# Performance work log

Measured on AMD Instinct MI355X. Metric: run time of the kernel, lower is better.

## Reference

```python
import jax, jax.numpy as jnp
import numpy as np

HEADS = 8
EMBED = 64
FEAT_A = 256
FEAT_B = 256


def setup_inputs() -> dict:
    key = jax.random.key(0)
    k1, k2, k3, k4, k5 = jax.random.split(key, 5)
    B, N = 2, 2048
    z_a = jax.random.normal(k1, (B, FEAT_A, N), dtype=jnp.float32)
    z_b = jax.random.normal(k2, (B, FEAT_B, N), dtype=jnp.float32)
    # Conv1d(k=1, bias=False) weights, squeezed: [out_ch, in_ch]
    W_a = jax.random.normal(k3, (HEADS * EMBED, FEAT_A), dtype=jnp.float32) * (1.0 / np.sqrt(FEAT_A))
    W_b = jax.random.normal(k4, (HEADS * EMBED, FEAT_B), dtype=jnp.float32) * (1.0 / np.sqrt(FEAT_B))
    W_c = jax.random.normal(k5, (FEAT_A, HEADS * FEAT_B), dtype=jnp.float32) * (1.0 / np.sqrt(HEADS * FEAT_B))
    return {"z_a": z_a, "z_b": z_b, "W_a": W_a, "W_b": W_b, "W_c": W_c}


def reference(z_a, z_b, W_a, W_b, W_c):
    B, Fa, Na = z_a.shape
    Fb = z_b.shape[1]
    H, E = HEADS, EMBED
    norm = 1.0 / np.sqrt(E)
    # 1x1 conv embeddings -> q, k: [B, H, E, N]
    q = jnp.einsum('of,bfn->bon', W_a, z_a).reshape(B, H, E, Na)
    k = jnp.einsum('of,bfn->bon', W_b, z_b).reshape(B, H, E, -1)
    v = z_b  # [B, Fb, K]
    # coeff_pre_softmax[b,h,q,k] = (q^T k) / sqrt(E)
    pre = jnp.einsum('bheq,bhek->bhqk', q, k) * norm
    coeff = jax.nn.softmax(pre, axis=-1)  # softmax over keys (dim=2 in torch bmm form)
    # l1 loss: mean |pre| over (q,k) per head, averaged over heads
    l1 = jnp.mean(jnp.abs(pre), axis=(1, 2, 3))  # [B]
    # feat[b,h,q,f] = coeff @ v^T
    feat = jnp.einsum('bhqk,bfk->bhqf', coeff, v)
    # combine heads: w[h] = W_c[:, h*Fb:(h+1)*Fb].T  -> [H, Fb, Fa]
    w = W_c.reshape(Fa, H, Fb).transpose(1, 2, 0)
    out = jnp.einsum('bhqf,hfo->bqo', feat, w)  # sum over heads
    return out, l1
```

## Files before the change

### kernel.cpp

```cpp
#include <hip/hip_runtime.h>
#include <hip/hip_bf16.h>


#define B_ 2
#define N_ 2048
#define F_ 256
#define H_ 8
#define E_ 64

typedef __attribute__((ext_vector_type(8))) short bf16x8;
typedef __attribute__((ext_vector_type(4))) float f32x4;

__device__ __forceinline__ unsigned short f2b(float x) {
  __hip_bfloat16 h = __float2bfloat16(x);
  return *reinterpret_cast<unsigned short*>(&h);
}

__device__ __forceinline__ unsigned short f2bt(float x) {
  union { float f; unsigned u; } c; c.f = x;
  return (unsigned short)(c.u >> 16);
}

__device__ __forceinline__ f32x4 mfma16(bf16x8 a, bf16x8 b, f32x4 c) {
  return __builtin_amdgcn_mfma_f32_16x16x32_bf16(a, b, c, 0, 0, 0);
}

__device__ __forceinline__ void async_lds16(const unsigned short* g, unsigned short* l) {
  __builtin_amdgcn_global_load_lds(
      (const __attribute__((address_space(1))) unsigned int*)g,
      (__attribute__((address_space(3))) unsigned int*)l, 16, 0, 0);
}

__global__ __launch_bounds__(256) void prep_kernel(
    const float* __restrict__ z_b, unsigned short* __restrict__ vbf,
    const float* __restrict__ W_c, unsigned short* __restrict__ wcb,
    const float* __restrict__ W_a, const float* __restrict__ W_b,
    unsigned short* __restrict__ wab, float* __restrict__ l1acc) {
  int i = blockIdx.x * 256 + threadIdx.x;
  if (i < B_) l1acc[i] = 0.f;
  const int nzb = B_ * F_ * N_ / 4;
  const int nwc = F_ * H_ * F_ / 4;
  const int nw = 512 * F_ / 4;
  const float* src; unsigned short* dst; int j;
  if (i < nzb) { src = z_b; dst = vbf; j = i; }
  else if (i < nzb + nwc) { src = W_c; dst = wcb; j = i - nzb; }
  else if (i < nzb + nwc + nw) { src = W_a; dst = wab; j = i - nzb - nwc; }
  else { j = i - nzb - nwc - nw; if (j >= nw) return; src = W_b; dst = wab + 512 * F_; }
  float4 v = reinterpret_cast<const float4*>(src)[j];
  unsigned long long pk =
      ((unsigned long long)f2b(v.w) << 48) | ((unsigned long long)f2b(v.z) << 32) |
      ((unsigned long long)f2b(v.y) << 16) | (unsigned long long)f2b(v.x);
  reinterpret_cast<unsigned long long*>(dst)[j] = pk;
}

__global__ __launch_bounds__(256) void transp_kernel(
    const float* __restrict__ z_a, const float* __restrict__ z_b,
    unsigned short* __restrict__ zaT, unsigned short* __restrict__ zbT) {
  __shared__ unsigned int t32[64][65];
  const int tid = threadIdx.x;
  const int nt = blockIdx.x, ft = blockIdx.y, wz = blockIdx.z;
  const int b = wz & 1, which = wz >> 1;
  const float* src = (which ? z_b : z_a) + (size_t)b * F_ * N_;
  unsigned short* dst = (which ? zbT : zaT) + (size_t)b * N_ * F_;
  const int col = tid & 63, rb = tid >> 6;
#pragma unroll
  for (int i = 0; i < 16; ++i) {
    int row = rb + i * 4;
    t32[row][col] = f2b(src[(size_t)(ft * 64 + row) * N_ + nt * 64 + col]);
  }
  __syncthreads();
#pragma unroll
  for (int i = 0; i < 16; ++i) {
    int row = rb + i * 4;
    dst[(size_t)(nt * 64 + row) * F_ + ft * 64 + col] = (unsigned short)t32[col][row];
  }
}

__global__ __launch_bounds__(256) void proj_mfma(
    const unsigned short* __restrict__ zaT, const unsigned short* __restrict__ zbT,
    const unsigned short* __restrict__ wab,
    unsigned short* __restrict__ qT, unsigned short* __restrict__ kT) {
  __shared__ __align__(16) unsigned short As[64][256];

  const int tid = threadIdx.x;
  const int wid = tid >> 6, lane = tid & 63;
  const int quad = lane >> 4, l16 = lane & 15;
  const int nt = blockIdx.x, ot = blockIdx.y, wz = blockIdx.z;
  const int b = wz & 1, which = wz >> 1;

  const unsigned short* zsrc = (which ? zbT : zaT) + (size_t)b * N_ * F_;
  const unsigned short* wsrc = wab + (size_t)which * 512 * F_;
  unsigned short* dst = (which ? kT : qT) + (size_t)b * N_ * 512;
  const float scale = which ? 1.f : 0.125f;

#pragma unroll
  for (int i = 0; i < 8; ++i) {
    int row = wid * 16 + 2 * i + (lane >> 5);
    int cg = (lane & 31) ^ (row & 31);
    async_lds16(zsrc + (size_t)(nt * 64 + row) * F_ + cg * 8, &As[wid * 16 + 2 * i][0]);
  }

  const unsigned short* brow = wsrc + (size_t)(ot * 64 + wid * 16 + l16) * F_ + quad * 8;

  f32x4 acc[4];
  const f32x4 zero4 = {0.f, 0.f, 0.f, 0.f};
#pragma unroll
  for (int g = 0; g < 4; ++g) acc[g] = zero4;

  __syncthreads();

#pragma unroll
  for (int kt = 0; kt < 8; ++kt) {
    bf16x8 bf = *reinterpret_cast<const bf16x8*>(brow + kt * 32);
#pragma unroll
    for (int g = 0; g < 4; ++g) {
      int row = g * 16 + l16;
      int p = (kt * 4 + quad) ^ (row & 31);
      bf16x8 af = *reinterpret_cast<const bf16x8*>(&As[0][0] + row * 256 + p * 8);
      acc[g] = mfma16(af, bf, acc[g]);
    }
  }

#pragma unroll
  for (int g = 0; g < 4; ++g)
#pragma unroll
    for (int r = 0; r < 4; ++r)
      dst[(size_t)(nt * 64 + g * 16 + quad * 4 + r) * 512 + ot * 64 + wid * 16 + l16] =
          f2b(acc[g][r] * scale);
}

__global__ __launch_bounds__(256, 3) void attn_mfma(
    const unsigned short* __restrict__ qT, const unsigned short* __restrict__ kT,
    const unsigned short* __restrict__ vbf, unsigned short* __restrict__ feat,
    float* __restrict__ l1acc) {
  __shared__ __align__(16) unsigned short ks[2][32][64];
  __shared__ __align__(16) unsigned short vs[2][256][32];
  __shared__ __align__(16) unsigned short p_blk[2][64][40];
  __shared__ float lsum_sh[64];
  __shared__ float redblk[256];

  const int tid = threadIdx.x;
  const int wid = tid >> 6, lane = tid & 63;
  const int quad = lane >> 4, l16 = lane & 15;
  const int qt = blockIdx.x, h = blockIdx.y, b = blockIdx.z;

  const int kkey = wid * 8 + (lane >> 3);
  const int kchunk = (lane & 7) ^ ((kkey >> 1) & 7);
  const unsigned short* kgl =
      kT + ((size_t)(b * N_ + kkey) * 512) + h * 64 + kchunk * 8;
  const unsigned short* vgl[4];
#pragma unroll
  for (int j = 0; j < 4; ++j) {
    int f = (wid * 4 + j) * 16 + (lane >> 2);
    int c = (lane & 3) ^ ((f >> 1) & 3);
    vgl[j] = vbf + ((size_t)(b * F_ + f) * 2048) + c * 8;
  }

  const unsigned short* qrow =
      qT + (size_t)(b * N_ + qt * 64 + wid * 16 + l16) * 512 + h * 64 + quad * 8;
  bf16x8 qf0 = *reinterpret_cast<const bf16x8*>(qrow);
  bf16x8 qf1 = *reinterpret_cast<const bf16x8*>(qrow + 32);

  const int koff = ((quad ^ (l16 & 7)) * 8);
  const int voff = ((quad ^ ((l16 >> 1) & 3)) * 8);

  f32x4 acc[4][4];
  const f32x4 zero4 = {0.f, 0.f, 0.f, 0.f};
#pragma unroll
  for (int g = 0; g < 4; ++g)
#pragma unroll
    for (int t = 0; t < 4; ++t) acc[g][t] = zero4;
  float lsum[4] = {0.f, 0.f, 0.f, 0.f};
  float suml1 = 0.f;
  bf16x8 vreg[4];

  async_lds16(kgl, &ks[0][wid * 8][0]);
#pragma unroll
  for (int j = 0; j < 4; ++j) async_lds16(vgl[j], &vs[0][(wid * 4 + j) * 16][0]);
  __syncthreads();

#pragma unroll 2
  for (int kt = 0; kt < N_ / 32; ++kt) {
    const int cur = kt & 1;
    if (kt + 1 < N_ / 32) {
      async_lds16(kgl + (size_t)(kt + 1) * 32 * 512, &ks[cur ^ 1][wid * 8][0]);
#pragma unroll
      for (int j = 0; j < 4; ++j)
        async_lds16(vgl[j] + (kt + 1) * 32, &vs[cur ^ 1][(wid * 4 + j) * 16][0]);
    }

    const unsigned short* ksc = &ks[cur][0][0];
    bf16x8 kf00 = *reinterpret_cast<const bf16x8*>(ksc + (2 * l16) * 64 + koff);
    bf16x8 kf01 = *reinterpret_cast<const bf16x8*>(ksc + (2 * l16) * 64 + (koff ^ 32));
    bf16x8 kf10 = *reinterpret_cast<const bf16x8*>(ksc + (2 * l16 + 1) * 64 + koff);
    bf16x8 kf11 = *reinterpret_cast<const bf16x8*>(ksc + (2 * l16 + 1) * 64 + (koff ^ 32));

    f32x4 s0 = mfma16(qf0, kf00, zero4); s0 = mfma16(qf1, kf01, s0);
    f32x4 s1 = mfma16(qf0, kf10, zero4); s1 = mfma16(qf1, kf11, s1);

#pragma unroll
    for (int r = 0; r < 4; ++r) {
      float a0 = s0[r], a1 = s1[r];
      suml1 += fabsf(a0) + fabsf(a1);
      float p0 = __expf(a0), p1 = __expf(a1);
      lsum[r] += p0 + p1;
      unsigned pk = ((unsigned)f2bt(p1) << 16) | f2bt(p0);
      *reinterpret_cast<unsigned*>(&p_blk[cur][wid * 16 + quad * 4 + r][2 * l16]) = pk;
    }

    if (kt > 0) {
#pragma unroll
      for (int g = 0; g < 4; ++g) {
        bf16x8 pf = *reinterpret_cast<const bf16x8*>(&p_blk[cur ^ 1][g * 16 + l16][quad * 8]);
#pragma unroll
        for (int t = 0; t < 4; ++t) acc[g][t] = mfma16(pf, vreg[t], acc[g][t]);
      }
    }

    {
      const unsigned short* vsc = &vs[cur][0][0];
#pragma unroll
      for (int t = 0; t < 4; ++t) {
        int f = wid * 64 + t * 16 + l16;
        vreg[t] = *reinterpret_cast<const bf16x8*>(vsc + f * 32 + voff);
      }
    }
    __syncthreads();
  }

  {
#pragma unroll
    for (int g = 0; g < 4; ++g) {
      bf16x8 pf = *reinterpret_cast<const bf16x8*>(&p_blk[1][g * 16 + l16][quad * 8]);
#pragma unroll
      for (int t = 0; t < 4; ++t) acc[g][t] = mfma16(pf, vreg[t], acc[g][t]);
    }
  }

#pragma unroll
  for (int r = 0; r < 4; ++r) {
    float rs = lsum[r];
    rs += __shfl_xor(rs, 1);
    rs += __shfl_xor(rs, 2);
    rs += __shfl_xor(rs, 4);
    rs += __shfl_xor(rs, 8);
    if (l16 == 0) lsum_sh[wid * 16 + quad * 4 + r] = rs;
  }
  __syncthreads();

#pragma unroll
  for (int g = 0; g < 4; ++g)
#pragma unroll
    for (int r = 0; r < 4; ++r) {
      float invl = 1.f / lsum_sh[g * 16 + quad * 4 + r];
      unsigned short* fr =
          feat + (size_t)(b * N_ + qt * 64 + g * 16 + quad * 4 + r) * 2048 +
          h * 256 + wid * 64 + l16;
#pragma unroll
      for (int t = 0; t < 4; ++t) fr[t * 16] = f2b(acc[g][t][r] * invl);
    }

  redblk[tid] = suml1;
  __syncthreads();
  for (int st = 128; st > 0; st >>= 1) {
    if (tid < st) redblk[tid] += redblk[tid + st];
    __syncthreads();
  }
  if (tid == 0) atomicAdd(&l1acc[b], redblk[0]);
}

__global__ __launch_bounds__(256) void combine_mfma(
    const unsigned short* __restrict__ feat, const unsigned short* __restrict__ wcb,
    const float* __restrict__ l1acc, float* __restrict__ out) {
  __shared__ __align__(16) unsigned short As[2][64][256];

  const int tid = threadIdx.x;
  const int wid = tid >> 6, lane = tid & 63;
  const int quad = lane >> 4, l16 = lane & 15;
  const int mb = blockIdx.x, ob = blockIdx.y;

  const int srow_hi = lane >> 5;
  const int spos = lane & 31;

  const unsigned short* brow = wcb + (size_t)(ob * 64 + wid * 16 + l16) * 2048 + quad * 8;

  f32x4 acc[4];
  const f32x4 zero4 = {0.f, 0.f, 0.f, 0.f};
#pragma unroll
  for (int g = 0; g < 4; ++g) acc[g] = zero4;

#pragma unroll
  for (int i = 0; i < 8; ++i) {
    int row = wid * 16 + 2 * i + srow_hi;
    int cg = spos ^ (row & 31);
    async_lds16(feat + (size_t)(mb * 64 + row) * 2048 + cg * 8, &As[0][wid * 16 + 2 * i][0]);
  }
  __syncthreads();

  for (int ch = 0; ch < 8; ++ch) {
    const int cur = ch & 1;
    if (ch + 1 < 8) {
#pragma unroll
      for (int i = 0; i < 8; ++i) {
        int row = wid * 16 + 2 * i + srow_hi;
        int cg = spos ^ (row & 31);
        async_lds16(feat + (size_t)(mb * 64 + row) * 2048 + (ch + 1) * 256 + cg * 8,
                    &As[cur ^ 1][wid * 16 + 2 * i][0]);
      }
    }
#pragma unroll
    for (int kt = 0; kt < 8; ++kt) {
      bf16x8 bf = *reinterpret_cast<const bf16x8*>(brow + ch * 256 + kt * 32);
#pragma unroll
      for (int g = 0; g < 4; ++g) {
        int row = g * 16 + l16;
        int p = (kt * 4 + quad) ^ (row & 31);
        bf16x8 af = *reinterpret_cast<const bf16x8*>(&As[cur][0][0] + row * 256 + p * 8);
        acc[g] = mfma16(af, bf, acc[g]);
      }
    }
    __syncthreads();
  }

#pragma unroll
  for (int g = 0; g < 4; ++g)
#pragma unroll
    for (int r = 0; r < 4; ++r)
      out[(size_t)(mb * 64 + g * 16 + quad * 4 + r) * 256 + ob * 64 + wid * 16 + l16] =
          acc[g][r];

  if (mb == 0 && ob == 0 && tid < B_)
    out[(size_t)B_ * N_ * F_ + tid] = l1acc[tid] * (1.f / (float)(H_ * N_ * N_));
}

extern "C" void kernel_launch(void* const* d_in, const int* in_sizes, int n_in,
                              void* d_out, int out_size, void* d_ws, size_t ws_size,
                              hipStream_t stream) {
  const float* z_a = (const float*)d_in[0];
  const float* z_b = (const float*)d_in[1];
  const float* W_a = (const float*)d_in[2];
  const float* W_b = (const float*)d_in[3];
  const float* W_c = (const float*)d_in[4];
  float* out = (float*)d_out;

  char* ws = (char*)d_ws;
  unsigned short* qT = (unsigned short*)ws;
  unsigned short* kT = (unsigned short*)(ws + ((size_t)4 << 20));
  unsigned short* vbf = (unsigned short*)(ws + ((size_t)8 << 20));
  unsigned short* wcb = (unsigned short*)(ws + ((size_t)10 << 20));
  unsigned short* zaT = (unsigned short*)(ws + ((size_t)11 << 20));
  unsigned short* zbT = (unsigned short*)(ws + ((size_t)13 << 20));
  unsigned short* wab = (unsigned short*)(ws + ((size_t)15 << 20));
  float* l1acc = (float*)(ws + ((size_t)15 << 20) + (768 << 10));
  unsigned short* feat = (unsigned short*)(ws + ((size_t)16 << 20));

  const int nprep = B_ * F_ * N_ / 4 + F_ * H_ * F_ / 4 + 2 * (512 * F_ / 4);
  prep_kernel<<<dim3((nprep + 255) / 256), 256, 0, stream>>>(
      z_b, vbf, W_c, wcb, W_a, W_b, wab, l1acc);
  transp_kernel<<<dim3(N_ / 64, F_ / 64, 4), 256, 0, stream>>>(z_a, z_b, zaT, zbT);
  proj_mfma<<<dim3(N_ / 64, 8, 4), 256, 0, stream>>>(zaT, zbT, wab, qT, kT);
  attn_mfma<<<dim3(N_ / 64, H_, B_), 256, 0, stream>>>(qT, kT, vbf, feat, l1acc);
  combine_mfma<<<dim3(B_ * N_ / 64, 4), 256, 0, stream>>>(feat, wcb, l1acc, out);
}
```

Measured before the change: 164.3 us.

## Triple-buffer K/V tiles with prefetch distance two and partial vmcnt waits

```diff
diff --git a/kernel.cpp b/kernel.cpp
--- a/kernel.cpp
+++ b/kernel.cpp
@@ -133,8 +133,8 @@
     const unsigned short* __restrict__ qT, const unsigned short* __restrict__ kT,
     const unsigned short* __restrict__ vbf, unsigned short* __restrict__ feat,
     float* __restrict__ l1acc) {
-  __shared__ __align__(16) unsigned short ks[2][32][64];
-  __shared__ __align__(16) unsigned short vs[2][256][32];
+  __shared__ __align__(16) unsigned short ks[3][32][64];
+  __shared__ __align__(16) unsigned short vs[3][256][32];
   __shared__ __align__(16) unsigned short p_blk[2][64][40];
   __shared__ float lsum_sh[64];
   __shared__ float redblk[256];
@@ -177,17 +177,25 @@
   async_lds16(kgl, &ks[0][wid * 8][0]);
 #pragma unroll
   for (int j = 0; j < 4; ++j) async_lds16(vgl[j], &vs[0][(wid * 4 + j) * 16][0]);
-  __syncthreads();
-
+  async_lds16(kgl + (size_t)32 * 512, &ks[1][wid * 8][0]);
+#pragma unroll
+  for (int j = 0; j < 4; ++j) async_lds16(vgl[j] + 32, &vs[1][(wid * 4 + j) * 16][0]);
+  asm volatile("s_waitcnt vmcnt(5)" ::: "memory");
+  __builtin_amdgcn_sched_barrier(0);
+  __builtin_amdgcn_s_barrier();
+  __builtin_amdgcn_sched_barrier(0);
+
+  int cur = 0, nx2 = 2;
 #pragma unroll 2
   for (int kt = 0; kt < N_ / 32; ++kt) {
-    const int cur = kt & 1;
-    if (kt + 1 < N_ / 32) {
-      async_lds16(kgl + (size_t)(kt + 1) * 32 * 512, &ks[cur ^ 1][wid * 8][0]);
+    if (kt + 2 < N_ / 32) {
+      async_lds16(kgl + (size_t)(kt + 2) * 32 * 512, &ks[nx2][wid * 8][0]);
 #pragma unroll
       for (int j = 0; j < 4; ++j)
-        async_lds16(vgl[j] + (kt + 1) * 32, &vs[cur ^ 1][(wid * 4 + j) * 16][0]);
-    }
+        async_lds16(vgl[j] + (kt + 2) * 32, &vs[nx2][(wid * 4 + j) * 16][0]);
+    }
+
+    const int pc = kt & 1;
 
     const unsigned short* ksc = &ks[cur][0][0];
     bf16x8 kf00 = *reinterpret_cast<const bf16x8*>(ksc + (2 * l16) * 64 + koff);
@@ -205,27 +213,42 @@
       float p0 = __expf(a0), p1 = __expf(a1);
       lsum[r] += p0 + p1;
       unsigned pk = ((unsigned)f2bt(p1) << 16) | f2bt(p0);
-      *reinterpret_cast<unsigned*>(&p_blk[cur][wid * 16 + quad * 4 + r][2 * l16]) = pk;
+      *reinterpret_cast<unsigned*>(&p_blk[pc][wid * 16 + quad * 4 + r][2 * l16]) = pk;
+    }
+
+    bf16x8 vnew[4];
+    {
+      const unsigned short* vsc = &vs[cur][0][0];
+#pragma unroll
+      for (int t = 0; t < 4; ++t) {
+        int f = wid * 64 + t * 16 + l16;
+        vnew[t] = *reinterpret_cast<const bf16x8*>(vsc + f * 32 + voff);
+      }
     }
 
     if (kt > 0) {
+      __builtin_amdgcn_s_setprio(1);
 #pragma unroll
       for (int g = 0; g < 4; ++g) {
-        bf16x8 pf = *reinterpret_cast<const bf16x8*>(&p_blk[cur ^ 1][g * 16 + l16][quad * 8]);
+        bf16x8 pf = *reinterpret_cast<const bf16x8*>(&p_blk[pc ^ 1][g * 16 + l16][quad * 8]);
 #pragma unroll
         for (int t = 0; t < 4; ++t) acc[g][t] = mfma16(pf, vreg[t], acc[g][t]);
       }
-    }
-
-    {
-      const unsigned short* vsc = &vs[cur][0][0];
-#pragma unroll
-      for (int t = 0; t < 4; ++t) {
-        int f = wid * 64 + t * 16 + l16;
-        vreg[t] = *reinterpret_cast<const bf16x8*>(vsc + f * 32 + voff);
-      }
-    }
-    __syncthreads();
+      __builtin_amdgcn_s_setprio(0);
+    }
+#pragma unroll
+    for (int t = 0; t < 4; ++t) vreg[t] = vnew[t];
+
+    if (kt < N_ / 32 - 2)
+      asm volatile("s_waitcnt vmcnt(5) lgkmcnt(0)" ::: "memory");
+    else
+      asm volatile("s_waitcnt vmcnt(0) lgkmcnt(0)" ::: "memory");
+    __builtin_amdgcn_sched_barrier(0);
+    __builtin_amdgcn_s_barrier();
+    __builtin_amdgcn_sched_barrier(0);
+
+    cur = (cur == 2) ? 0 : cur + 1;
+    nx2 = (nx2 == 2) ? 0 : nx2 + 1;
   }
 
   {
```

Measured after the change: 175.8 us. 7.0% more time.
